# Kernel optimization log

Measured on AMD Instinct MI355X. Metric: run time of the kernel, lower is better.

The kernel has to match this reference:

```python
import jax, jax.numpy as jnp
import numpy as np

T, B, D, H, O = 1024, 64, 256, 512, 256


def setup_inputs() -> dict:
    key = jax.random.key(0)
    ks = jax.random.split(key, 4)
    s_i = 1.0 / np.sqrt(D)
    s_h = 1.0 / np.sqrt(H)
    return {
        "x": jax.random.normal(ks[0], (T, B, D), jnp.float32),
        "Wi": jax.random.normal(ks[1], (D, 3 * H), jnp.float32) * s_i,
        "bi": jnp.zeros((3 * H,), jnp.float32),
        "Wh": jax.random.normal(ks[2], (H, 3 * H), jnp.float32) * s_h,
        "bhn": jnp.zeros((H,), jnp.float32),
        "Wo": jax.random.normal(ks[3], (H, O), jnp.float32) * s_h,
        "bo": jnp.zeros((O,), jnp.float32),
        "h0": jnp.zeros((B, H), jnp.float32),
    }


def reference(x, Wi, bi, Wh, bhn, Wo, bo, h0):
    # Precompute all input-to-gate projections at once: [T, B, 3H]
    xg = jnp.einsum('tbd,dg->tbg', x, Wi) + bi

    def step(h, xg_t):
        hg = h @ Wh                      # [B, 3H]
        xr, xz, xn = jnp.split(xg_t, 3, axis=-1)
        hr, hz, hn = jnp.split(hg, 3, axis=-1)
        r = jax.nn.sigmoid(xr + hr)
        z = jax.nn.sigmoid(xz + hz)
        n = jnp.tanh(xn + r * (hn + bhn))
        h_new = (1.0 - z) * n + z * h
        return h_new, h_new

    _, hs = jax.lax.scan(step, h0, xg)   # hs: [T, B, H]
    out = jnp.einsum('tbh,ho->tbo', hs, Wo) + bo  # per-step readout
    return out
```

## Files before the change

kernel.cpp:

```cpp
#include <hip/hip_runtime.h>


#define T_ 1024
#define B_ 64
#define D_ 256
#define H_ 512
#define G_ 1536
#define O_ 256

#define SENT 0x7FC0u

typedef __attribute__((ext_vector_type(8))) short short8;
typedef __attribute__((ext_vector_type(4))) short short4v;
typedef __attribute__((ext_vector_type(4))) float float4v;
typedef __attribute__((ext_vector_type(4))) unsigned int uint4v;

static __device__ __forceinline__ unsigned short f2b(float f) {
  unsigned u = __builtin_bit_cast(unsigned, f);
  u += 0x7fffu + ((u >> 16) & 1u);
  return (unsigned short)(u >> 16);
}

__global__ __launch_bounds__(256) void prep_kernel(
    const float* __restrict__ x, const float* __restrict__ Wi,
    const float* __restrict__ Wh, const float* __restrict__ Wo,
    unsigned short* __restrict__ xb, unsigned short* __restrict__ WhT,
    unsigned short* __restrict__ WiT, unsigned short* __restrict__ WoT,
    unsigned short* __restrict__ hs)
{
  const size_t NX4 = (size_t)T_ * B_ * D_ / 4;
  const size_t NWH = (size_t)G_ * H_;
  const size_t NWI = (size_t)G_ * D_;
  const size_t NWO = (size_t)O_ * H_;
  const size_t NH8 = (size_t)T_ * B_ * H_ / 8;
  const size_t NTOT = NX4 + NWH + NWI + NWO + NH8;
  size_t i = (size_t)blockIdx.x * blockDim.x + threadIdx.x;
  const size_t stride = (size_t)gridDim.x * blockDim.x;
  for (; i < NTOT; i += stride) {
    if (i < NX4) {
      float4v f = ((const float4v*)x)[i];
      short4v o;
      o[0] = (short)f2b(f[0]); o[1] = (short)f2b(f[1]);
      o[2] = (short)f2b(f[2]); o[3] = (short)f2b(f[3]);
      ((short4v*)xb)[i] = o;
      continue;
    }
    size_t j = i - NX4;
    if (j < NWH) { size_t g = j >> 9, k = j & 511; WhT[j] = f2b(Wh[k * G_ + g]); continue; }
    j -= NWH;
    if (j < NWI) { size_t g = j >> 8, k = j & 255; WiT[j] = f2b(Wi[k * G_ + g]); continue; }
    j -= NWI;
    if (j < NWO) { size_t o = j >> 9, k = j & 511; WoT[j] = f2b(Wo[k * O_ + o]); continue; }
    j -= NWO;
    uint4v sv = {0x7FC07FC0u, 0x7FC07FC0u, 0x7FC07FC0u, 0x7FC07FC0u};
    ((uint4v*)hs)[j] = sv;
  }
}

__global__ __launch_bounds__(384, 2) void scan_kernel(
    const unsigned short* __restrict__ xb,
    const unsigned short* __restrict__ WhT,
    const unsigned short* __restrict__ WiT,
    unsigned short* __restrict__ hs,
    const float* __restrict__ bi,
    const float* __restrict__ bhn,
    const float* __restrict__ h0)
{
  const int wg = blockIdx.x;
  const int group = wg & 3;
  const int slice = wg >> 2;
  const int tid = threadIdx.x;
  const int wave = tid >> 6;
  const int lane = tid & 63;
  const int m = lane & 15;
  const int quad = lane >> 4;
  const int gk = wave % 3;
  const int s = wave / 3;
  const int row0 = group * 16;
  const int jbase = slice * 32 + s * 16;
  const int gcol = gk * 512 + jbase + m;

  __shared__ unsigned short hT[16 * 512];
  struct HX { float h, x; };
  __shared__ HX lds_hx[6][256];
  __shared__ unsigned short h_out[16 * 32];

  short8 Bh[16], Bx[8];
  {
    const unsigned short* p = WhT + (size_t)gcol * H_ + quad * 8;
#pragma unroll
    for (int k = 0; k < 16; ++k) Bh[k] = *(const short8*)(p + k * 32);
    const unsigned short* q = WiT + (size_t)gcol * D_ + quad * 8;
#pragma unroll
    for (int k = 0; k < 8; ++k) Bx[k] = *(const short8*)(q + k * 32);
  }

  const int jcol = jbase + m;
  const float bi_r = bi[jcol];
  const float bi_z = bi[512 + jcol];
  const float bi_n = bi[1024 + jcol];
  const float bhn_c = bhn[jcol];
  float hold[4];
#pragma unroll
  for (int i = 0; i < 4; ++i)
    hold[i] = h0[(size_t)(row0 + quad * 4 + i) * H_ + jcol];

  for (int i = tid; i < 16 * 512; i += 384) {
    int r = i >> 9, c = i & 511;
    int c2 = (((c >> 3) ^ (r & 7)) << 3) | (c & 7);
    hT[r * 512 + c2] = f2b(h0[(size_t)(row0 + r) * H_ + c]);
  }
  float4v accx = {0.f, 0.f, 0.f, 0.f};
  {
    const unsigned short* xp = xb + ((size_t)0 * B_ + row0 + m) * D_ + quad * 8;
#pragma unroll
    for (int k = 0; k < 8; ++k)
      accx = __builtin_amdgcn_mfma_f32_16x16x32_bf16(*(const short8*)(xp + k * 32), Bx[k], accx, 0, 0, 0);
  }
  __syncthreads();

  for (int t = 0; t < T_; ++t) {
    float4v acch0 = {0.f, 0.f, 0.f, 0.f}, acch1 = {0.f, 0.f, 0.f, 0.f};
#pragma unroll
    for (int k = 0; k < 16; k += 2) {
      const int blk0 = (k * 4 + quad) ^ (m & 7);
      short8 a0 = *(const short8*)&hT[m * 512 + blk0 * 8];
      acch0 = __builtin_amdgcn_mfma_f32_16x16x32_bf16(a0, Bh[k], acch0, 0, 0, 0);
      const int blk1 = ((k + 1) * 4 + quad) ^ (m & 7);
      short8 a1 = *(const short8*)&hT[m * 512 + blk1 * 8];
      acch1 = __builtin_amdgcn_mfma_f32_16x16x32_bf16(a1, Bh[k + 1], acch1, 0, 0, 0);
    }
#pragma unroll
    for (int i = 0; i < 4; ++i) {
      const int idx = (quad * 4 + i) * 16 + m;
      HX v; v.h = acch0[i] + acch1[i]; v.x = accx[i];
      lds_hx[wave][idx] = v;
    }
    __syncthreads();
    if (gk == 0) {
      const int wb = s * 3;
#pragma unroll
      for (int i = 0; i < 4; ++i) {
        const int r = quad * 4 + i;
        const int idx = r * 16 + m;
        const HX vr = lds_hx[wb + 0][idx];
        const HX vz = lds_hx[wb + 1][idx];
        const HX vn = lds_hx[wb + 2][idx];
        const float pr = vr.h + vr.x + bi_r;
        const float pz = vz.h + vz.x + bi_z;
        const float rg = 1.f / (1.f + __expf(-pr));
        const float zg = 1.f / (1.f + __expf(-pz));
        const float an = vn.x + bi_n + rg * (vn.h + bhn_c);
        const float e2 = __expf(2.f * an);
        const float ng = 1.f - 2.f / (e2 + 1.f);
        const float hn = (1.f - zg) * ng + zg * hold[i];
        hold[i] = hn;
        h_out[r * 32 + s * 16 + m] = f2b(hn);
      }
    }
    short8 xa[8];
    if (t < T_ - 1) {
      const unsigned short* xp = xb + ((size_t)(t + 1) * B_ + row0 + m) * D_ + quad * 8;
#pragma unroll
      for (int k = 0; k < 8; ++k) xa[k] = *(const short8*)(xp + k * 32);
    }
    __syncthreads();
    if (wave == 1) {
      const int r = lane >> 2, c8 = (lane & 3) * 8;
      short8 hv = *(const short8*)&h_out[r * 32 + c8];
      unsigned short* dst = hs + ((size_t)t * B_ + row0 + r) * H_ + slice * 32 + c8;
      asm volatile("global_store_dwordx4 %0, %1, off sc0 sc1"
                   :: "v"(dst), "v"(hv) : "memory");
    }
    if (t < T_ - 1) {
      const unsigned short* src = hs + ((size_t)t * B_ + row0) * H_;
      const int c0 = tid, c1 = tid + 384;
      const int c2r = tid + 768;
      const int c2 = (c2r < 1024) ? c2r : c0;
      const short8* p0 = (const short8*)(src + (size_t)c0 * 8);
      const short8* p1 = (const short8*)(src + (size_t)c1 * 8);
      const short8* p2 = (const short8*)(src + (size_t)c2 * 8);
      short8 v0, v1, v2;
      bool bad;
      do {
        asm volatile(
            "global_load_dwordx4 %0, %3, off sc0 sc1\n\t"
            "global_load_dwordx4 %1, %4, off sc0 sc1\n\t"
            "global_load_dwordx4 %2, %5, off sc0 sc1\n\t"
            "s_waitcnt vmcnt(0)"
            : "=&v"(v0), "=&v"(v1), "=&v"(v2)
            : "v"(p0), "v"(p1), "v"(p2));
        bad = false;
#pragma unroll
        for (int e = 0; e < 8; ++e) {
          bad |= ((unsigned short)v0[e] == (unsigned short)SENT);
          bad |= ((unsigned short)v1[e] == (unsigned short)SENT);
          bad |= ((unsigned short)v2[e] == (unsigned short)SENT);
        }
      } while (bad);
      { const int r = c0 >> 6, b2 = (c0 & 63) ^ (r & 7); *(short8*)&hT[r * 512 + b2 * 8] = v0; }
      { const int r = c1 >> 6, b2 = (c1 & 63) ^ (r & 7); *(short8*)&hT[r * 512 + b2 * 8] = v1; }
      if (c2r < 1024) { const int r = c2r >> 6, b2 = (c2r & 63) ^ (r & 7); *(short8*)&hT[r * 512 + b2 * 8] = v2; }
      float4v ax0 = {0.f, 0.f, 0.f, 0.f}, ax1 = {0.f, 0.f, 0.f, 0.f};
#pragma unroll
      for (int k = 0; k < 8; k += 2) {
        ax0 = __builtin_amdgcn_mfma_f32_16x16x32_bf16(xa[k], Bx[k], ax0, 0, 0, 0);
        ax1 = __builtin_amdgcn_mfma_f32_16x16x32_bf16(xa[k + 1], Bx[k + 1], ax1, 0, 0, 0);
      }
#pragma unroll
      for (int i = 0; i < 4; ++i) accx[i] = ax0[i] + ax1[i];
      __syncthreads();
    }
  }
}

__global__ __launch_bounds__(256) void ogemm_kernel(
    const unsigned short* __restrict__ hs, const unsigned short* __restrict__ WoT,
    const float* __restrict__ bo, float* __restrict__ out)
{
  const int wv = threadIdx.x >> 6, lane = threadIdx.x & 63;
  const int m = lane & 15, quad = lane >> 4;
  const int rowbase = blockIdx.x * 64 + wv * 16;
  const unsigned short* ap = hs + (size_t)(rowbase + m) * H_ + quad * 8;
  float4v acc[16];
#pragma unroll
  for (int n = 0; n < 16; ++n) { float4v z = {0.f,0.f,0.f,0.f}; acc[n] = z; }
#pragma unroll
  for (int k = 0; k < 16; ++k) {
    short8 a = *(const short8*)(ap + k * 32);
#pragma unroll
    for (int n = 0; n < 16; ++n) {
      short8 b = *(const short8*)(WoT + (size_t)(n * 16 + m) * H_ + k * 32 + quad * 8);
      acc[n] = __builtin_amdgcn_mfma_f32_16x16x32_bf16(a, b, acc[n], 0, 0, 0);
    }
  }
#pragma unroll
  for (int n = 0; n < 16; ++n) {
    const int col = n * 16 + m;
    const float bias = bo[col];
#pragma unroll
    for (int i = 0; i < 4; ++i) {
      const int r = rowbase + quad * 4 + i;
      out[(size_t)r * O_ + col] = acc[n][i] + bias;
    }
  }
}

extern "C" void kernel_launch(void* const* d_in, const int* in_sizes, int n_in,
                              void* d_out, int out_size, void* d_ws, size_t ws_size,
                              hipStream_t stream)
{
  const float* x   = (const float*)d_in[0];
  const float* Wi  = (const float*)d_in[1];
  const float* bi  = (const float*)d_in[2];
  const float* Wh  = (const float*)d_in[3];
  const float* bhn = (const float*)d_in[4];
  const float* Wo  = (const float*)d_in[5];
  const float* bo  = (const float*)d_in[6];
  const float* h0  = (const float*)d_in[7];
  float* out = (float*)d_out;

  char* ws = (char*)d_ws;
  unsigned short* xb  = (unsigned short*)ws;  ws += (size_t)T_ * B_ * D_ * 2;
  unsigned short* WhT = (unsigned short*)ws;  ws += (size_t)G_ * H_ * 2;
  unsigned short* WiT = (unsigned short*)ws;  ws += (size_t)G_ * D_ * 2;
  unsigned short* WoT = (unsigned short*)ws;  ws += (size_t)O_ * H_ * 2;
  unsigned short* hs  = (unsigned short*)ws;

  prep_kernel<<<4096, 256, 0, stream>>>(x, Wi, Wh, Wo, xb, WhT, WiT, WoT, hs);
  scan_kernel<<<64, 384, 0, stream>>>(xb, WhT, WiT, hs, bi, bhn, h0);
  ogemm_kernel<<<1024, 256, 0, stream>>>(hs, WoT, bo, out);
}
```

Baseline: 3.272 ms.

## Detect same-XCC groups and use L2-coherent loads/stores instead of system scope

The scan launches twice as many workgroups and keeps only groups 0-3 out of every 8. With round-robin XCC dispatch this should place each batch group's 16 slices on a single XCC. Each workgroup reads its XCC ID and publishes it to a buffer; if all 16 slices of its group sit on the same XCC, the cross-workgroup hidden-state exchange uses sc0-only loads and stores, which are coherent in the shared L2, instead of sc0 sc1 system-scope traffic. This is meant to cut the latency of the per-step polling handshake. It depends on the dispatch-to-XCC mapping and falls back to the coherent path when that mapping does not hold.

```diff
diff --git a/kernel.cpp b/kernel.cpp
--- a/kernel.cpp
+++ b/kernel.cpp
@@ -26,14 +26,15 @@
     const float* __restrict__ Wh, const float* __restrict__ Wo,
     unsigned short* __restrict__ xb, unsigned short* __restrict__ WhT,
     unsigned short* __restrict__ WiT, unsigned short* __restrict__ WoT,
-    unsigned short* __restrict__ hs)
+    unsigned short* __restrict__ hs, unsigned* __restrict__ xccbuf)
 {
   const size_t NX4 = (size_t)T_ * B_ * D_ / 4;
   const size_t NWH = (size_t)G_ * H_;
   const size_t NWI = (size_t)G_ * D_;
   const size_t NWO = (size_t)O_ * H_;
   const size_t NH8 = (size_t)T_ * B_ * H_ / 8;
-  const size_t NTOT = NX4 + NWH + NWI + NWO + NH8;
+  const size_t NXC = 128;
+  const size_t NTOT = NX4 + NWH + NWI + NWO + NH8 + NXC;
   size_t i = (size_t)blockIdx.x * blockDim.x + threadIdx.x;
   const size_t stride = (size_t)gridDim.x * blockDim.x;
   for (; i < NTOT; i += stride) {
@@ -52,8 +53,13 @@
     j -= NWI;
     if (j < NWO) { size_t o = j >> 9, k = j & 511; WoT[j] = f2b(Wo[k * O_ + o]); continue; }
     j -= NWO;
-    uint4v sv = {0x7FC07FC0u, 0x7FC07FC0u, 0x7FC07FC0u, 0x7FC07FC0u};
-    ((uint4v*)hs)[j] = sv;
+    if (j < NH8) {
+      uint4v sv = {0x7FC07FC0u, 0x7FC07FC0u, 0x7FC07FC0u, 0x7FC07FC0u};
+      ((uint4v*)hs)[j] = sv;
+      continue;
+    }
+    j -= NH8;
+    xccbuf[j] = 0u;
   }
 }
 
@@ -64,11 +70,13 @@
     unsigned short* __restrict__ hs,
     const float* __restrict__ bi,
     const float* __restrict__ bhn,
-    const float* __restrict__ h0)
+    const float* __restrict__ h0,
+    unsigned* __restrict__ xccbuf)
 {
   const int wg = blockIdx.x;
-  const int group = wg & 3;
-  const int slice = wg >> 2;
+  const int group = wg & 7;
+  if (group >= 4) return;
+  const int slice = wg >> 3;
   const int tid = threadIdx.x;
   const int wave = tid >> 6;
   const int lane = tid & 63;
@@ -84,6 +92,7 @@
   struct HX { float h, x; };
   __shared__ HX lds_hx[6][256];
   __shared__ unsigned short h_out[16 * 32];
+  __shared__ int fast_lds;
 
   short8 Bh[16], Bx[8];
   {
@@ -117,7 +126,32 @@
     for (int k = 0; k < 8; ++k)
       accx = __builtin_amdgcn_mfma_f32_16x16x32_bf16(*(const short8*)(xp + k * 32), Bx[k], accx, 0, 0, 0);
   }
+
+  {
+    unsigned xcc;
+    asm("s_getreg_b32 %0, hwreg(HW_REG_XCC_ID)" : "=s"(xcc));
+    if (tid == 0) {
+      unsigned tok = xcc + 1u;
+      unsigned* slot = xccbuf + wg;
+      asm volatile("global_store_dword %0, %1, off sc0 sc1"
+                   :: "v"(slot), "v"(tok) : "memory");
+    }
+    if (wave == 0) {
+      unsigned v = 0xffffffffu;
+      if (lane < 16) {
+        const unsigned* p = xccbuf + group + 8 * lane;
+        do {
+          asm volatile("global_load_dword %0, %1, off sc0 sc1\n\t"
+                       "s_waitcnt vmcnt(0)" : "=&v"(v) : "v"(p));
+        } while (v == 0u);
+      }
+      unsigned ref = __shfl(v, 0, 64);
+      bool ok = (lane < 16) ? (v == ref) : true;
+      if (lane == 0) fast_lds = (__ballot(ok) == ~0ull) ? 1 : 0;
+    }
+  }
   __syncthreads();
+  const bool fast = (fast_lds != 0);
 
   for (int t = 0; t < T_; ++t) {
     float4v acch0 = {0.f, 0.f, 0.f, 0.f}, acch1 = {0.f, 0.f, 0.f, 0.f};
@@ -169,8 +203,12 @@
       const int r = lane >> 2, c8 = (lane & 3) * 8;
       short8 hv = *(const short8*)&h_out[r * 32 + c8];
       unsigned short* dst = hs + ((size_t)t * B_ + row0 + r) * H_ + slice * 32 + c8;
-      asm volatile("global_store_dwordx4 %0, %1, off sc0 sc1"
-                   :: "v"(dst), "v"(hv) : "memory");
+      if (fast)
+        asm volatile("global_store_dwordx4 %0, %1, off sc0"
+                     :: "v"(dst), "v"(hv) : "memory");
+      else
+        asm volatile("global_store_dwordx4 %0, %1, off sc0 sc1"
+                     :: "v"(dst), "v"(hv) : "memory");
     }
     if (t < T_ - 1) {
       const unsigned short* src = hs + ((size_t)t * B_ + row0) * H_;
@@ -182,22 +220,41 @@
       const short8* p2 = (const short8*)(src + (size_t)c2 * 8);
       short8 v0, v1, v2;
       bool bad;
-      do {
-        asm volatile(
-            "global_load_dwordx4 %0, %3, off sc0 sc1\n\t"
-            "global_load_dwordx4 %1, %4, off sc0 sc1\n\t"
-            "global_load_dwordx4 %2, %5, off sc0 sc1\n\t"
-            "s_waitcnt vmcnt(0)"
-            : "=&v"(v0), "=&v"(v1), "=&v"(v2)
-            : "v"(p0), "v"(p1), "v"(p2));
-        bad = false;
-#pragma unroll
-        for (int e = 0; e < 8; ++e) {
-          bad |= ((unsigned short)v0[e] == (unsigned short)SENT);
-          bad |= ((unsigned short)v1[e] == (unsigned short)SENT);
-          bad |= ((unsigned short)v2[e] == (unsigned short)SENT);
-        }
-      } while (bad);
+      if (fast) {
+        do {
+          asm volatile(
+              "global_load_dwordx4 %0, %3, off sc0\n\t"
+              "global_load_dwordx4 %1, %4, off sc0\n\t"
+              "global_load_dwordx4 %2, %5, off sc0\n\t"
+              "s_waitcnt vmcnt(0)"
+              : "=&v"(v0), "=&v"(v1), "=&v"(v2)
+              : "v"(p0), "v"(p1), "v"(p2));
+          bad = false;
+#pragma unroll
+          for (int e = 0; e < 8; ++e) {
+            bad |= ((unsigned short)v0[e] == (unsigned short)SENT);
+            bad |= ((unsigned short)v1[e] == (unsigned short)SENT);
+            bad |= ((unsigned short)v2[e] == (unsigned short)SENT);
+          }
+        } while (bad);
+      } else {
+        do {
+          asm volatile(
+              "global_load_dwordx4 %0, %3, off sc0 sc1\n\t"
+              "global_load_dwordx4 %1, %4, off sc0 sc1\n\t"
+              "global_load_dwordx4 %2, %5, off sc0 sc1\n\t"
+              "s_waitcnt vmcnt(0)"
+              : "=&v"(v0), "=&v"(v1), "=&v"(v2)
+              : "v"(p0), "v"(p1), "v"(p2));
+          bad = false;
+#pragma unroll
+          for (int e = 0; e < 8; ++e) {
+            bad |= ((unsigned short)v0[e] == (unsigned short)SENT);
+            bad |= ((unsigned short)v1[e] == (unsigned short)SENT);
+            bad |= ((unsigned short)v2[e] == (unsigned short)SENT);
+          }
+        } while (bad);
+      }
       { const int r = c0 >> 6, b2 = (c0 & 63) ^ (r & 7); *(short8*)&hT[r * 512 + b2 * 8] = v0; }
       { const int r = c1 >> 6, b2 = (c1 & 63) ^ (r & 7); *(short8*)&hT[r * 512 + b2 * 8] = v1; }
       if (c2r < 1024) { const int r = c2r >> 6, b2 = (c2r & 63) ^ (r & 7); *(short8*)&hT[r * 512 + b2 * 8] = v2; }
@@ -265,9 +322,10 @@
   unsigned short* WhT = (unsigned short*)ws;  ws += (size_t)G_ * H_ * 2;
   unsigned short* WiT = (unsigned short*)ws;  ws += (size_t)G_ * D_ * 2;
   unsigned short* WoT = (unsigned short*)ws;  ws += (size_t)O_ * H_ * 2;
-  unsigned short* hs  = (unsigned short*)ws;
-
-  prep_kernel<<<4096, 256, 0, stream>>>(x, Wi, Wh, Wo, xb, WhT, WiT, WoT, hs);
-  scan_kernel<<<64, 384, 0, stream>>>(xb, WhT, WiT, hs, bi, bhn, h0);
+  unsigned short* hs  = (unsigned short*)ws;  ws += (size_t)T_ * B_ * H_ * 2;
+  unsigned* xccbuf    = (unsigned*)ws;
+
+  prep_kernel<<<4096, 256, 0, stream>>>(x, Wi, Wh, Wo, xb, WhT, WiT, WoT, hs, xccbuf);
+  scan_kernel<<<128, 384, 0, stream>>>(xb, WhT, WiT, hs, bi, bhn, h0, xccbuf);
   ogemm_kernel<<<1024, 256, 0, stream>>>(hs, WoT, bo, out);
 }
```

After: 3.178 ms. -2.9%, faster.
